# Performance work log

Measured on AMD Instinct MI355X. Metric: run time of the kernel, lower is better.

The kernel has to match this reference:

```python
import jax, jax.numpy as jnp
import numpy as np

HIDDEN_DIM = 1024
NUM_HEADS = 16
HEAD_DIM = HIDDEN_DIM // NUM_HEADS
SCALAR_NORM = float(np.sqrt(HIDDEN_DIM / NUM_HEADS))


def setup_inputs() -> dict:
    key = jax.random.key(0)
    k1, k2 = jax.random.split(key)
    B, N, D = 2, 2048, HIDDEN_DIM
    x = jax.random.normal(k1, (B, N, D), dtype=jnp.float32)
    # torch Linear weight shape: (3D, D); xavier_uniform-like scale
    limit = float(np.sqrt(6.0 / (D + 3 * D)))
    W_qkv = jax.random.uniform(k2, (3 * D, D), dtype=jnp.float32, minval=-limit, maxval=limit)
    return {"x": x, "W_qkv": W_qkv}


def reference(x, W_qkv):
    b, n, d = x.shape
    h, hd = NUM_HEADS, HEAD_DIM
    qkv = x @ W_qkv.T  # (B, N, 3D)
    q, k, v = jnp.split(qkv, 3, axis=-1)
    # (B, H, N, hd)
    q = q.reshape(b, n, h, hd).transpose(0, 2, 1, 3)
    k = k.reshape(b, n, h, hd).transpose(0, 2, 1, 3)
    v = v.reshape(b, n, h, hd).transpose(0, 2, 1, 3)
    scores = jnp.einsum('bhik,bhjk->bhij', q, k) / SCALAR_NORM
    attn = jax.nn.softmax(scores, axis=-1)
    out = jnp.einsum('bhij,bhjk->bhik', attn, v)
    return out.transpose(0, 2, 1, 3).reshape(b, n, d)
```

## Files before the change

kernel.cpp:

```cpp
#include <hip/hip_runtime.h>
#include <hip/hip_bf16.h>

#define SEQ 2048
#define DMODEL 1024
#define NHEADS 16
#define HD 64
#define BATCH 2

typedef short bf16x8 __attribute__((ext_vector_type(8)));
typedef float f32x4 __attribute__((ext_vector_type(4)));
typedef float f32x16 __attribute__((ext_vector_type(16)));

static __device__ inline ushort f2bf(float f) {
    unsigned u = __float_as_uint(f);
    return (ushort)((u + 0x7fffu + ((u >> 16) & 1u)) >> 16);
}

static __device__ inline unsigned pk2bf(float a, float b) {
    __hip_bfloat162 h = __float22bfloat162_rn(make_float2(a, b));
    union { __hip_bfloat162 h; unsigned u; } c; c.h = h;
    return c.u;
}

static __device__ inline void async16(const ushort* g, ushort* l) {
    __builtin_amdgcn_global_load_lds((const __attribute__((address_space(1))) void*)g,
                                     (__attribute__((address_space(3))) void*)l, 16, 0, 0);
}

static __device__ inline void plane32swap(unsigned& a, unsigned& b) {
    asm volatile("v_permlane32_swap_b32 %0, %1" : "+v"(a), "+v"(b));
}

__global__ void cvt2(const float* __restrict__ a, ushort* __restrict__ da, int na,
                     const float* __restrict__ b, ushort* __restrict__ db, int nb) {
    long i = (long)(blockIdx.x * blockDim.x + threadIdx.x) * 4;
    const float* s; ushort* d;
    if (i < na) { s = a + i; d = da + i; }
    else { long j = i - na; if (j >= nb) return; s = b + j; d = db + j; }
    float4 v = *(const float4*)s;
    ushort4 o; o.x = f2bf(v.x); o.y = f2bf(v.y); o.z = f2bf(v.z); o.w = f2bf(v.w);
    *(ushort4*)d = o;
}

union GemmSmem {
    struct { ushort A[128 * 64]; ushort B[128 * 64]; } st;
    ushort C[128 * 128];
};

__global__ __launch_bounds__(256) void qkv_gemm(
        const ushort* __restrict__ X, const ushort* __restrict__ W,
        ushort* __restrict__ Qd, ushort* __restrict__ Kd, ushort* __restrict__ Vd) {
    __shared__ GemmSmem sm;
    const int t = threadIdx.x;
    const int lane = t & 63, l15 = lane & 15, quad = lane >> 4;
    const int w = t >> 6, wm = w >> 1, wn = w & 1;
    const int gm = blockIdx.x, gn = blockIdx.y;
    const int srow = t >> 3, scol = (t & 7) * 8;

    f32x4 acc[4][4] = {};

    for (int kt = 0; kt < 16; ++kt) {
        const int k0 = kt * 64;
        __syncthreads();
#pragma unroll
        for (int inst = 0; inst < 4; ++inst) {
            async16(&X[(gm * 128 + inst * 32 + srow) * 1024 + k0 + scol], &sm.st.A[inst * 2048 + t * 8]);
            async16(&W[(gn * 128 + inst * 32 + srow) * 1024 + k0 + scol], &sm.st.B[inst * 2048 + t * 8]);
        }
        __syncthreads();
#pragma unroll
        for (int ks = 0; ks < 2; ++ks) {
            const int kk = ks * 32 + quad * 8;
            bf16x8 af[4], bfr[4];
#pragma unroll
            for (int i = 0; i < 4; ++i) {
                af[i]  = *(const bf16x8*)&sm.st.A[(wm * 64 + i * 16 + l15) * 64 + kk];
                bfr[i] = *(const bf16x8*)&sm.st.B[(wn * 64 + i * 16 + l15) * 64 + kk];
            }
#pragma unroll
            for (int i = 0; i < 4; ++i)
#pragma unroll
                for (int j = 0; j < 4; ++j)
                    acc[i][j] = __builtin_amdgcn_mfma_f32_16x16x32_bf16(af[i], bfr[j], acc[i][j], 0, 0, 0);
        }
    }

    __syncthreads();
    if (gn < 16) {
        const float sc = (gn < 8) ? (0.125f * 1.44269504f) : 1.0f;
#pragma unroll
        for (int i = 0; i < 4; ++i)
#pragma unroll
            for (int reg = 0; reg < 4; ++reg) {
                const int row = wm * 64 + i * 16 + quad * 4 + reg;
                const int sw = (row & 7) * 8;
#pragma unroll
                for (int jp = 0; jp < 4; jp += 2) {
                    unsigned u = pk2bf(acc[i][jp][reg] * sc, acc[i][jp + 1][reg] * sc);
                    sm.C[row * 128 + ((wn * 64 + jp * 16 + l15) ^ sw)] = (ushort)u;
                    sm.C[row * 128 + ((wn * 64 + (jp + 1) * 16 + l15) ^ sw)] = (ushort)(u >> 16);
                }
            }
        __syncthreads();

        ushort* dst = (gn < 8) ? Qd : Kd;
        const int rloc = t >> 4, l = t & 15;
#pragma unroll
        for (int pass = 0; pass < 8; ++pass) {
            const int r = pass * 16 + rloc;
            bf16x8 v = *(const bf16x8*)&sm.C[r * 128 + ((l * 8) ^ ((r & 7) * 8))];
            const int ng = gm * 128 + r;
            const int b = ng >> 11, n = ng & 2047;
            const int cl = (gn * 128 + l * 8) & 1023;
            const int h = cl >> 6, hd = cl & 63;
            *(bf16x8*)&dst[(((b * NHEADS + h) * SEQ) + n) * HD + hd] = v;
        }
    } else {
#pragma unroll
        for (int i = 0; i < 4; ++i)
#pragma unroll
            for (int reg = 0; reg < 4; ++reg) {
                const int nloc = wm * 64 + i * 16 + quad * 4 + reg;
#pragma unroll
                for (int jp = 0; jp < 4; ++jp) {
                    const int f = wn * 64 + jp * 16 + l15;
                    sm.C[f * 128 + (nloc ^ ((f & 7) * 8))] = f2bf(acc[i][jp][reg]);
                }
            }
        __syncthreads();

        const int rloc = t >> 4, l = t & 15;
        const int b = gm >> 4;
        const int n0 = (gm & 15) * 128 + l * 8;
#pragma unroll
        for (int pass = 0; pass < 8; ++pass) {
            const int r = pass * 16 + rloc;
            bf16x8 v = *(const bf16x8*)&sm.C[r * 128 + ((l * 8) ^ ((r & 7) * 8))];
            const int cl = (gn * 128 + r) & 1023;
            const int h = cl >> 6, hd = cl & 63;
            *(bf16x8*)&Vd[(((long)(b * NHEADS + h) * HD) + hd) * SEQ + n0] = v;
        }
    }
}

__global__ __launch_bounds__(256, 1) void attn_kernel(
        const ushort* __restrict__ Q, const ushort* __restrict__ K,
        const ushort* __restrict__ VT, float* __restrict__ O) {
    __shared__ ushort sK[2][128 * 64];
    __shared__ ushort sVT[2][64 * 128];
    __shared__ float sL[4][64];

    const int t = threadIdx.x;
    const int lane = t & 63, l31 = lane & 31, hi = lane >> 5;
    const int w = t >> 6;

    const int flat = blockIdx.y * gridDim.x + blockIdx.x;
    const int qt = (flat >> 3) & 7;
    const int bh = (flat & 7) + ((flat >> 6) << 3);

    const ushort* Qp = Q + ((long)bh * SEQ + qt * 256 + w * 64) * HD;
    const ushort* Kp = K + (long)bh * SEQ * HD;
    const ushort* Vp = VT + (long)bh * HD * SEQ;

    bf16x8 bq[2][4];
#pragma unroll
    for (int qh = 0; qh < 2; ++qh)
#pragma unroll
        for (int ks = 0; ks < 4; ++ks)
            bq[qh][ks] = *(const bf16x8*)&Qp[(qh * 32 + l31) * HD + ks * 16 + hi * 8];

    const int krow = t >> 3;
    const int kcol = ((t & 7) ^ (krow & 7)) * 8;
    const ushort* gK = Kp + krow * HD + kcol;
    const int vrow = t >> 4;
    const int vcol = ((t & 15) ^ (vrow & 7)) * 8;
    const ushort* gV = Vp + (long)vrow * SEQ + vcol;

    ushort* lK[2] = { &sK[0][t * 8], &sK[1][t * 8] };
    ushort* lV[2] = { &sVT[0][t * 8], &sVT[1][t * 8] };

    f32x16 accA[2] = {}, accB[2] = {};
    f32x4 LpA = {}, LpB = {};
    const int swz = (l31 & 7) << 3;

#pragma unroll
    for (int c = 0; c < 4; ++c) {
        async16(gK + c * 32 * HD, lK[0] + c * 2048);
        async16(gV + (long)c * 16 * SEQ, lV[0] + c * 2048);
    }
    __syncthreads();

    for (int kt = 0; kt < 16; ++kt) {
        const int cur = kt & 1;
        if (kt < 15) {
            const ushort* nK = gK + (kt + 1) * 128 * HD;
            const ushort* nV = gV + (kt + 1) * 128;
#pragma unroll
            for (int c = 0; c < 4; ++c) {
                async16(nK + c * 32 * HD, lK[cur ^ 1] + c * 2048);
                async16(nV + (long)c * 16 * SEQ, lV[cur ^ 1] + c * 2048);
            }
        }
        const ushort* bK = sK[cur];
        const ushort* bV = sVT[cur];

        f32x16 sA[4], sB[4];
#pragma unroll
        for (int nb = 0; nb < 4; ++nb) {
            f32x16 zA = {}, zB = {};
#pragma unroll
            for (int ks = 0; ks < 4; ++ks) {
                bf16x8 ak = *(const bf16x8*)&bK[(nb * 32 + l31) * 64 + ((ks * 16 + hi * 8) ^ swz)];
                zA = __builtin_amdgcn_mfma_f32_32x32x16_bf16(ak, bq[0][ks], zA, 0, 0, 0);
                zB = __builtin_amdgcn_mfma_f32_32x32x16_bf16(ak, bq[1][ks], zB, 0, 0, 0);
            }
            sA[nb] = zA; sB[nb] = zB;
        }

#pragma unroll
        for (int h = 0; h < 2; ++h) {
            bf16x8 paA[4], paB[4];
#pragma unroll
            for (int nb2 = 0; nb2 < 2; ++nb2) {
                float pA[16], pB[16];
#pragma unroll
                for (int r = 0; r < 16; ++r) {
                    pA[r] = __builtin_amdgcn_exp2f(sA[h * 2 + nb2][r]);
                    pB[r] = __builtin_amdgcn_exp2f(sB[h * 2 + nb2][r]);
                }
#pragma unroll
                for (int r = 0; r < 16; ++r) { LpA[r & 3] += pA[r]; LpB[r & 3] += pB[r]; }
#pragma unroll
                for (int h2 = 0; h2 < 2; ++h2) {
                    const int b = 8 * h2;
                    unsigned a0 = pk2bf(pA[b + 0], pA[b + 1]);
                    unsigned a1 = pk2bf(pA[b + 2], pA[b + 3]);
                    unsigned a2 = pk2bf(pA[b + 4], pA[b + 5]);
                    unsigned a3 = pk2bf(pA[b + 6], pA[b + 7]);
                    plane32swap(a0, a2);
                    plane32swap(a1, a3);
                    union { unsigned u[4]; bf16x8 v; } fa;
                    fa.u[0] = a0; fa.u[1] = a1; fa.u[2] = a2; fa.u[3] = a3;
                    paA[nb2 * 2 + h2] = fa.v;
                    unsigned b0 = pk2bf(pB[b + 0], pB[b + 1]);
                    unsigned b1 = pk2bf(pB[b + 2], pB[b + 3]);
                    unsigned b2 = pk2bf(pB[b + 4], pB[b + 5]);
                    unsigned b3 = pk2bf(pB[b + 6], pB[b + 7]);
                    plane32swap(b0, b2);
                    plane32swap(b1, b3);
                    union { unsigned u[4]; bf16x8 v; } fb;
                    fb.u[0] = b0; fb.u[1] = b1; fb.u[2] = b2; fb.u[3] = b3;
                    paB[nb2 * 2 + h2] = fb.v;
                }
            }
#pragma unroll
            for (int db = 0; db < 2; ++db)
#pragma unroll
                for (int ks = 0; ks < 4; ++ks) {
                    bf16x8 vf = *(const bf16x8*)&bV[(db * 32 + l31) * 128 + h * 64 + ((ks * 16 + hi * 8) ^ swz)];
                    accA[db] = __builtin_amdgcn_mfma_f32_32x32x16_bf16(paA[ks], vf, accA[db], 0, 0, 0);
                    accB[db] = __builtin_amdgcn_mfma_f32_32x32x16_bf16(paB[ks], vf, accB[db], 0, 0, 0);
                }
        }

        __syncthreads();
    }

    {
        const float la = (LpA[0] + LpA[1]) + (LpA[2] + LpA[3]);
        unsigned lu = __float_as_uint(la), lv = lu;
        plane32swap(lu, lv);
        const float lb = (LpB[0] + LpB[1]) + (LpB[2] + LpB[3]);
        unsigned mu = __float_as_uint(lb), mv = mu;
        plane32swap(mu, mv);
        if (hi == 0) {
            sL[w][l31]      = __uint_as_float(lu) + __uint_as_float(lv);
            sL[w][32 + l31] = __uint_as_float(mu) + __uint_as_float(mv);
        }
    }
    __syncthreads();

    const int b = bh >> 4, h = bh & 15;
    const int qg0 = qt * 256 + w * 64;
#pragma unroll
    for (int r = 0; r < 16; ++r) {
        const int ql = (r & 3) + 8 * (r >> 2) + 4 * hi;
        const float invA = 1.0f / sL[w][ql];
        const float invB = 1.0f / sL[w][32 + ql];
#pragma unroll
        for (int db = 0; db < 2; ++db) {
            O[((long)b * SEQ + qg0 + ql) * DMODEL + h * HD + db * 32 + l31]      = accA[db][r] * invA;
            O[((long)b * SEQ + qg0 + 32 + ql) * DMODEL + h * HD + db * 32 + l31] = accB[db][r] * invB;
        }
    }
}

extern "C" void kernel_launch(void* const* d_in, const int* in_sizes, int n_in,
                              void* d_out, int out_size, void* d_ws, size_t ws_size,
                              hipStream_t stream) {
    const float* x  = (const float*)d_in[0];
    const float* Wq = (const float*)d_in[1];
    float* out = (float*)d_out;

    const int NX = BATCH * SEQ * DMODEL;
    const int NW = 3 * DMODEL * DMODEL;
    const int NQKV = BATCH * NHEADS * SEQ * HD;

    ushort* xb = (ushort*)d_ws;
    ushort* wb = xb + NX;
    ushort* q  = wb + NW;
    ushort* k  = q + NQKV;
    ushort* vt = k + NQKV;

    cvt2<<<(NX + NW) / 4 / 256, 256, 0, stream>>>(x, xb, NX, Wq, wb, NW);

    dim3 g1(4096 / 128, 3072 / 128);
    qkv_gemm<<<g1, 256, 0, stream>>>(xb, wb, q, k, vt);

    dim3 g2(SEQ / 256, BATCH * NHEADS);
    attn_kernel<<<g2, 256, 0, stream>>>(q, k, vt, out);
}
```

Before: 175.2 us.

## Double-buffer QKV GEMM LDS tiles and XOR-swizzle them to avoid bank conflicts

The QKV projection GEMM now keeps two LDS stage buffers. It issues the async global-to-LDS loads for the next K tile before running the MFMAs on the current one, and needs only one barrier per iteration instead of two. The tile columns are also XOR-swizzled by row on store and load, to cut LDS bank conflicts on the bf16x8 fragment reads. The cost is doubling the staging LDS to 64 KB per block, which may lower occupancy.

```diff
diff --git a/kernel.cpp b/kernel.cpp
--- a/kernel.cpp
+++ b/kernel.cpp
@@ -43,7 +43,7 @@
 }
 
 union GemmSmem {
-    struct { ushort A[128 * 64]; ushort B[128 * 64]; } st;
+    struct { ushort A[128 * 64]; ushort B[128 * 64]; } st[2];
     ushort C[128 * 128];
 };
 
@@ -55,27 +55,40 @@
     const int lane = t & 63, l15 = lane & 15, quad = lane >> 4;
     const int w = t >> 6, wm = w >> 1, wn = w & 1;
     const int gm = blockIdx.x, gn = blockIdx.y;
-    const int srow = t >> 3, scol = (t & 7) * 8;
+
+    const int srow = t >> 3;
+    const int scol = ((t & 7) ^ (srow & 7)) * 8;
+    const ushort* gA = &X[(gm * 128 + srow) * 1024 + scol];
+    const ushort* gB = &W[(gn * 128 + srow) * 1024 + scol];
 
     f32x4 acc[4][4] = {};
 
+    auto stage = [&](int kt, int buf) {
+        ushort* A = sm.st[buf].A;
+        ushort* B = sm.st[buf].B;
+#pragma unroll
+        for (int i = 0; i < 4; ++i) {
+            async16(gA + i * 32 * 1024 + kt * 64, &A[i * 2048 + t * 8]);
+            async16(gB + i * 32 * 1024 + kt * 64, &B[i * 2048 + t * 8]);
+        }
+    };
+
+    stage(0, 0);
+    __syncthreads();
+
     for (int kt = 0; kt < 16; ++kt) {
-        const int k0 = kt * 64;
-        __syncthreads();
-#pragma unroll
-        for (int inst = 0; inst < 4; ++inst) {
-            async16(&X[(gm * 128 + inst * 32 + srow) * 1024 + k0 + scol], &sm.st.A[inst * 2048 + t * 8]);
-            async16(&W[(gn * 128 + inst * 32 + srow) * 1024 + k0 + scol], &sm.st.B[inst * 2048 + t * 8]);
-        }
-        __syncthreads();
+        const int buf = kt & 1;
+        if (kt < 15) stage(kt + 1, buf ^ 1);
+        const ushort* A = sm.st[buf].A;
+        const ushort* B = sm.st[buf].B;
 #pragma unroll
         for (int ks = 0; ks < 2; ++ks) {
-            const int kk = ks * 32 + quad * 8;
+            const int off = ((ks * 4 + quad) ^ (l15 & 7)) * 8;
             bf16x8 af[4], bfr[4];
 #pragma unroll
             for (int i = 0; i < 4; ++i) {
-                af[i]  = *(const bf16x8*)&sm.st.A[(wm * 64 + i * 16 + l15) * 64 + kk];
-                bfr[i] = *(const bf16x8*)&sm.st.B[(wn * 64 + i * 16 + l15) * 64 + kk];
+                af[i]  = *(const bf16x8*)&A[(wm * 64 + i * 16 + l15) * 64 + off];
+                bfr[i] = *(const bf16x8*)&B[(wn * 64 + i * 16 + l15) * 64 + off];
             }
 #pragma unroll
             for (int i = 0; i < 4; ++i)
@@ -83,9 +96,9 @@
                 for (int j = 0; j < 4; ++j)
                     acc[i][j] = __builtin_amdgcn_mfma_f32_16x16x32_bf16(af[i], bfr[j], acc[i][j], 0, 0, 0);
         }
-    }
-
-    __syncthreads();
+        __syncthreads();
+    }
+
     if (gn < 16) {
         const float sc = (gn < 8) ? (0.125f * 1.44269504f) : 1.0f;
 #pragma unroll
```

Measured after the change: 159.8 us. 1.1x faster.
